# Optimization experiments

Measured on AMD Instinct MI355X. Metric: run time of the kernel, lower is better.

Reference implementation:

```python
import jax, jax.numpy as jnp
import numpy as np

N = 50000        # nodes
E = 800000       # edges (before self-loops)
NFEAT = 256
NHID = 32
HEADS = 8
NOUT = 128
NEG_SLOPE = 0.2
EPS = 1e-5


def _gat_layer(x, src, dst, W, att_src, att_dst, bias, heads, ch, concat):
    """PyG-style GATConv (shared weights for src/dst, self-loops already appended)."""
    n = x.shape[0]
    h = (x @ W).reshape(n, heads, ch)                      # [N,H,C]
    a_src = (h * att_src).sum(-1)                          # [N,H]
    a_dst = (h * att_dst).sum(-1)                          # [N,H]
    e = jax.nn.leaky_relu(a_src[src] + a_dst[dst], NEG_SLOPE)  # [E',H]
    # segment softmax over incoming edges of each dst node
    m = jax.ops.segment_max(e, dst, num_segments=n)        # [N,H]
    m = jnp.where(jnp.isfinite(m), m, 0.0)
    ex = jnp.exp(e - m[dst])                               # [E',H]
    denom = jax.ops.segment_sum(ex, dst, num_segments=n)   # [N,H]
    alpha = ex / (denom[dst] + 1e-16)                      # [E',H]
    msg = h[src] * alpha[:, :, None]                       # [E',H,C]
    out = jax.ops.segment_sum(msg, dst, num_segments=n)    # [N,H,C]
    out = out.reshape(n, heads * ch) if concat else out.mean(axis=1)
    return out + bias


def setup_inputs() -> dict:
    key = jax.random.key(0)
    ks = jax.random.split(key, 14)
    s = 0.05
    return {
        "x": jax.random.normal(ks[0], (N, NFEAT), jnp.float32),
        "edge_index": jax.random.randint(ks[1], (2, E), 0, N, dtype=jnp.int64),
        "W1": jax.random.normal(ks[2], (NFEAT, HEADS * NHID), jnp.float32) * s,
        "att_src1": jax.random.normal(ks[3], (HEADS, NHID), jnp.float32) * s,
        "att_dst1": jax.random.normal(ks[4], (HEADS, NHID), jnp.float32) * s,
        "b1": jnp.zeros((HEADS * NHID,), jnp.float32),
        "W2": jax.random.normal(ks[5], (HEADS * NHID, NOUT), jnp.float32) * s,
        "att_src2": jax.random.normal(ks[6], (1, NOUT), jnp.float32) * s,
        "att_dst2": jax.random.normal(ks[7], (1, NOUT), jnp.float32) * s,
        "b2": jnp.zeros((NOUT,), jnp.float32),
        "bn_gamma": jnp.ones((NOUT,), jnp.float32),
        "bn_beta": jnp.zeros((NOUT,), jnp.float32),
        "ln_gamma": jnp.ones((NOUT,), jnp.float32),
        "ln_beta": jnp.zeros((NOUT,), jnp.float32),
    }


def reference(x, edge_index, W1, att_src1, att_dst1, b1, W2, att_src2, att_dst2, b2,
              bn_gamma, bn_beta, ln_gamma, ln_beta):
    loops = jnp.arange(N, dtype=edge_index.dtype)
    src = jnp.concatenate([edge_index[0], loops])
    dst = jnp.concatenate([edge_index[1], loops])
    # layer 1: concat heads, then relu (dropout is identity at inference)
    h = jax.nn.relu(_gat_layer(x, src, dst, W1, att_src1, att_dst1, b1, HEADS, NHID, True))
    # layer 2: single head, mean (no concat), relu
    h = jax.nn.relu(_gat_layer(h, src, dst, W2, att_src2, att_dst2, b2, 1, NOUT, False))
    # BatchNorm1d with batch statistics (biased var, eps=1e-5)
    mu = h.mean(axis=0)
    var = h.var(axis=0)
    h = (h - mu) / jnp.sqrt(var + EPS) * bn_gamma + bn_beta
    # LayerNorm over last dim
    mu2 = h.mean(axis=-1, keepdims=True)
    var2 = h.var(axis=-1, keepdims=True)
    return (h - mu2) / jnp.sqrt(var2 + EPS) * ln_gamma + ln_beta
```

## Files before the change

kernel.cpp:

```cpp
#include <hip/hip_runtime.h>
#include <cstdint>
#include <cstddef>

#define HEADS   8
#define NFEAT   256
#define NOUT    128
#define NEG     0.2f
#define EPSV    1e-5f

typedef unsigned short ushort_t;
typedef __attribute__((ext_vector_type(8))) short s8v;
typedef __attribute__((ext_vector_type(4))) float f4v;

static __device__ __forceinline__ float lrelu(float x) { return x > 0.f ? x : NEG * x; }

static __device__ __forceinline__ float bf2f(ushort_t u) {
    union { unsigned int i; float f; } v; v.i = ((unsigned int)u) << 16; return v.f;
}
static __device__ __forceinline__ ushort_t f2bf(float f) {
    union { float f; unsigned int i; } v; v.f = f;
    unsigned int x = v.i;
    return (ushort_t)((x + 0x7fff + ((x >> 16) & 1)) >> 16);
}
static __device__ __forceinline__ float bits2f(unsigned int u) {
    union { unsigned int i; float f; } v; v.i = u; return v.f;
}
static __device__ __forceinline__ unsigned int f2bits(float f) {
    union { float f; unsigned int i; } v; v.f = f; return v.i;
}

static __device__ __forceinline__ int detect64(const int* __restrict__ ei, int E) {
    int lane = threadIdx.x & 63;
    long idx = 2L * ((long)lane * (E / 64)) + 1;
    int v = ei[idx];
    unsigned long long ball = __ballot(v == 0);
    return (ball == ~0ull) ? 1 : 0;
}

__global__ void k_count(const int* __restrict__ ei, int* __restrict__ counts,
                        int E, int n) {
    int is64 = detect64(ei, E);
    int i = blockIdx.x * blockDim.x + threadIdx.x;
    if (i < E) {
        int d = ei[(size_t)(E + i) << is64];
        atomicAdd(&counts[d], 1);
    } else if (i < E + n) {
        atomicAdd(&counts[i - E], 1);
    }
}

__global__ __launch_bounds__(1024) void k_scan1(const int* __restrict__ counts,
                                                int* __restrict__ incl,
                                                int* __restrict__ bsum, int n) {
    int t = threadIdx.x, i = blockIdx.x * 1024 + t;
    int lane = t & 63, w = t >> 6;
    int v = (i < n) ? counts[i] : 0;
    int sv = v;
#pragma unroll
    for (int o = 1; o < 64; o <<= 1) { int u = __shfl_up(sv, o, 64); if (lane >= o) sv += u; }
    __shared__ int wsum[16];
    if (lane == 63) wsum[w] = sv;
    __syncthreads();
    if (w == 0) {
        int bs = (lane < 16) ? wsum[lane] : 0;
#pragma unroll
        for (int o = 1; o < 16; o <<= 1) { int u = __shfl_up(bs, o, 64); if (lane >= o) bs += u; }
        if (lane < 16) wsum[lane] = bs;
    }
    __syncthreads();
    int pre = (w > 0) ? wsum[w - 1] : 0;
    sv += pre;
    if (i < n) incl[i] = sv;
    if (t == 1023) bsum[blockIdx.x] = sv;
}

__global__ void k_scan3(const int* __restrict__ incl, const int* __restrict__ bsum,
                        const int* __restrict__ counts,
                        int* __restrict__ offs, int* __restrict__ cursor, int n) {
    __shared__ int pre_s;
    int chunk = blockIdx.x >> 2;
    if (threadIdx.x == 0) {
        int s = 0;
        for (int j = 0; j < chunk; ++j) s += bsum[j];
        pre_s = s;
    }
    __syncthreads();
    int i = blockIdx.x * 256 + threadIdx.x;
    if (i < n) {
        int v = incl[i] + pre_s;
        offs[i + 1] = v;
        cursor[i] = v - counts[i];
    }
    if (i == 0) offs[0] = 0;
}

__global__ void k_fill(const int* __restrict__ ei, int* __restrict__ cursor,
                       int* __restrict__ esrc, int E, int n) {
    int is64 = detect64(ei, E);
    int i = blockIdx.x * blockDim.x + threadIdx.x;
    if (i >= E + n) return;
    int s, d;
    if (i < E) { s = ei[(size_t)i << is64]; d = ei[(size_t)(E + i) << is64]; }
    else       { s = i - E; d = s; }
    int p = atomicAdd(&cursor[d], 1);
    esrc[p] = s;
}

__global__ void k_prepw(const float* __restrict__ W1, const float* __restrict__ W2,
                        ushort_t* __restrict__ Wh1, ushort_t* __restrict__ Wl1,
                        ushort_t* __restrict__ Wh2, ushort_t* __restrict__ Wl2) {
    int gid = blockIdx.x * 256 + threadIdx.x;
    const float* W; ushort_t* Wh; ushort_t* Wl; int M;
    if (gid < 256 * 256) { W = W1; Wh = Wh1; Wl = Wl1; M = 256; }
    else { gid -= 256 * 256; if (gid >= 256 * 128) return; W = W2; Wh = Wh2; Wl = Wl2; M = 128; }
    int k = gid / M, nn = gid - k * M;
    int ntile = nn >> 4, j = nn & 15, kc = k >> 3, e = k & 7;
    int p = ((ntile * 32 + kc) * 16 + j) * 8 + e;
    float v = W[(size_t)k * M + nn];
    ushort_t hi = f2bf(v);
    float r = v - bf2f(hi);
    Wh[p] = hi;
    Wl[p] = f2bf(r);
}

__global__ __launch_bounds__(256) void k_mm(const float* __restrict__ A,
                                            const ushort_t* __restrict__ Wh,
                                            const ushort_t* __restrict__ Wl,
                                            ushort_t* __restrict__ C, int n, int Mout) {
    __shared__ ushort_t Ah[128][40];
    __shared__ ushort_t Al[128][40];
    const int t = threadIdx.x;
    const int lane = t & 63, w = t >> 6;
    const int wr = w >> 1, wc = w & 1;
    const int r0 = blockIdx.x * 128;
    const int srow = t >> 1;
    const int kh = (t & 1) * 16;
    const int arow = r0 + srow;
    const bool rowok = arow < n;

    f4v acc[4][4];
#pragma unroll
    for (int a = 0; a < 4; ++a)
#pragma unroll
        for (int b = 0; b < 4; ++b) { f4v z = {0.f, 0.f, 0.f, 0.f}; acc[a][b] = z; }

    float pre[16];
    const float* abase = &A[(size_t)arow * 256 + kh];
#pragma unroll
    for (int q = 0; q < 4; ++q) {
        float4 v = rowok ? *reinterpret_cast<const float4*>(abase + q * 4)
                         : float4{0.f, 0.f, 0.f, 0.f};
        pre[q * 4 + 0] = v.x; pre[q * 4 + 1] = v.y;
        pre[q * 4 + 2] = v.z; pre[q * 4 + 3] = v.w;
    }

    const int lj = lane & 15, lk = lane >> 4;

    for (int kb = 0; kb < 256; kb += 32) {
        __syncthreads();
#pragma unroll
        for (int q = 0; q < 2; ++q) {
            unsigned int hw[4], lw[4];
#pragma unroll
            for (int p = 0; p < 4; ++p) {
                unsigned int x0 = f2bits(pre[q * 8 + p * 2]);
                unsigned int x1 = f2bits(pre[q * 8 + p * 2 + 1]);
                unsigned int h1b = x1 & 0xffff0000u;
                float lo0 = bits2f(f2bits(pre[q * 8 + p * 2])) - bits2f(x0 & 0xffff0000u);
                float lo1 = pre[q * 8 + p * 2 + 1] - bits2f(h1b);
                hw[p] = (x0 >> 16) | h1b;
                lw[p] = (f2bits(lo0) >> 16) | (f2bits(lo1) & 0xffff0000u);
            }
            uint4 hv = {hw[0], hw[1], hw[2], hw[3]};
            uint4 lv = {lw[0], lw[1], lw[2], lw[3]};
            *reinterpret_cast<uint4*>(&Ah[srow][kh + q * 8]) = hv;
            *reinterpret_cast<uint4*>(&Al[srow][kh + q * 8]) = lv;
        }
        __syncthreads();
        if (kb < 224) {
            const float* ap = abase + kb + 32;
#pragma unroll
            for (int q = 0; q < 4; ++q) {
                float4 v = rowok ? *reinterpret_cast<const float4*>(ap + q * 4)
                                 : float4{0.f, 0.f, 0.f, 0.f};
                pre[q * 4 + 0] = v.x; pre[q * 4 + 1] = v.y;
                pre[q * 4 + 2] = v.z; pre[q * 4 + 3] = v.w;
            }
        }
        const int kc0 = kb >> 3;
        s8v ah[4], al[4];
#pragma unroll
        for (int mf = 0; mf < 4; ++mf) {
            ah[mf] = *reinterpret_cast<const s8v*>(&Ah[wr * 64 + mf * 16 + lj][lk * 8]);
            al[mf] = *reinterpret_cast<const s8v*>(&Al[wr * 64 + mf * 16 + lj][lk * 8]);
        }
#pragma unroll
        for (int nf = 0; nf < 4; ++nf) {
            int ntile = blockIdx.y * 8 + wc * 4 + nf;
            size_t boff = ((size_t)(ntile * 32 + kc0 + lk) * 16 + lj) * 8;
            s8v bh = *reinterpret_cast<const s8v*>(&Wh[boff]);
            s8v bl = *reinterpret_cast<const s8v*>(&Wl[boff]);
#pragma unroll
            for (int mf = 0; mf < 4; ++mf) {
                acc[mf][nf] = __builtin_amdgcn_mfma_f32_16x16x32_bf16(ah[mf], bh, acc[mf][nf], 0, 0, 0);
                acc[mf][nf] = __builtin_amdgcn_mfma_f32_16x16x32_bf16(ah[mf], bl, acc[mf][nf], 0, 0, 0);
                acc[mf][nf] = __builtin_amdgcn_mfma_f32_16x16x32_bf16(al[mf], bh, acc[mf][nf], 0, 0, 0);
            }
        }
    }

#pragma unroll
    for (int mf = 0; mf < 4; ++mf) {
        int rr = r0 + wr * 64 + mf * 16 + lk * 4;
#pragma unroll
        for (int nf = 0; nf < 4; ++nf) {
            int cc = blockIdx.y * 128 + wc * 64 + nf * 16 + lj;
#pragma unroll
            for (int r = 0; r < 4; ++r) {
                if (rr + r < n) C[(size_t)(rr + r) * Mout + cc] = f2bf(acc[mf][nf][r]);
            }
        }
    }
}

__global__ __launch_bounds__(256) void k_att1(const ushort_t* __restrict__ h1,
                                              const float* __restrict__ att_s,
                                              const float* __restrict__ att_d,
                                              float* __restrict__ as1,
                                              float* __restrict__ ad1, int n) {
    int wid = (blockIdx.x * blockDim.x + threadIdx.x) >> 6;
    int lane = threadIdx.x & 63;
    if (wid >= n) return;
    int head = lane >> 3;
    int co = (lane & 7) * 4;
    ushort4 hu = *reinterpret_cast<const ushort4*>(&h1[(size_t)wid * 256 + head * 32 + co]);
    float4 vs = *reinterpret_cast<const float4*>(&att_s[head * 32 + co]);
    float4 vd = *reinterpret_cast<const float4*>(&att_d[head * 32 + co]);
    float hx = bf2f(hu.x), hy = bf2f(hu.y), hz = bf2f(hu.z), hw = bf2f(hu.w);
    float ss = hx * vs.x + hy * vs.y + hz * vs.z + hw * vs.w;
    float sd = hx * vd.x + hy * vd.y + hz * vd.z + hw * vd.w;
#pragma unroll
    for (int o = 1; o < 8; o <<= 1) { ss += __shfl_xor(ss, o, 64); sd += __shfl_xor(sd, o, 64); }
    if ((lane & 7) == 0) {
        as1[(size_t)wid * 8 + head] = ss;
        ad1[(size_t)wid * 8 + head] = sd;
    }
}

__global__ __launch_bounds__(256) void k_att2(const ushort_t* __restrict__ h2,
                                              const float* __restrict__ att_s,
                                              const float* __restrict__ att_d,
                                              float* __restrict__ as2,
                                              float* __restrict__ ad2, int n) {
    int wid = (blockIdx.x * blockDim.x + threadIdx.x) >> 6;
    int lane = threadIdx.x & 63;
    if (wid >= n) return;
    ushort2 hu = *reinterpret_cast<const ushort2*>(&h2[(size_t)wid * 128 + lane * 2]);
    float2 vs = *reinterpret_cast<const float2*>(&att_s[lane * 2]);
    float2 vd = *reinterpret_cast<const float2*>(&att_d[lane * 2]);
    float hx = bf2f(hu.x), hy = bf2f(hu.y);
    float ss = hx * vs.x + hy * vs.y;
    float sd = hx * vd.x + hy * vd.y;
#pragma unroll
    for (int o = 1; o < 64; o <<= 1) { ss += __shfl_xor(ss, o, 64); sd += __shfl_xor(sd, o, 64); }
    if (lane == 0) { as2[wid] = ss; ad2[wid] = sd; }
}

__global__ __launch_bounds__(256) void k_agg1(const ushort_t* __restrict__ h1,
                                              const float* __restrict__ as1,
                                              const float* __restrict__ ad1,
                                              const int* __restrict__ offs,
                                              const int* __restrict__ esrc,
                                              const float* __restrict__ b1,
                                              float* __restrict__ out1, int n, int tot) {
    int wid = (blockIdx.x * blockDim.x + threadIdx.x) >> 6;
    int lane = threadIdx.x & 63;
    if (wid >= n) return;
    int e0 = offs[wid], e1 = offs[wid + 1];
    int deg = e1 - e0;

    if (deg <= 64) {
        const int l = lane & 31;
        const int h = lane >> 5;
        const int hd = l >> 2;
        const int cb = l * 8;

        int ei_idx = e0 + lane;
        int es = esrc[ei_idx < tot ? ei_idx : (tot - 1)];

        const int headA = lane >> 3, g = lane & 7;
        float adnA = ad1[(size_t)wid * 8 + headA];
        float a[8];
#pragma unroll
        for (int k = 0; k < 8; ++k) {
            int i = g + 8 * k;
            int s = __shfl(es, i, 64);
            a[k] = (i < deg) ? as1[(size_t)s * 8 + headA] : -1e30f;
        }
        float mx = a[0];
#pragma unroll
        for (int k = 1; k < 8; ++k) mx = fmaxf(mx, a[k]);
#pragma unroll
        for (int o = 1; o < 8; o <<= 1) mx = fmaxf(mx, __shfl_xor(mx, o, 64));
        float mA = lrelu(mx + adnA);
#pragma unroll
        for (int k = 0; k < 8; ++k)
            a[k] = __expf(lrelu(a[k] + adnA) - mA);

        float d = 0.f;
        float ac0 = 0.f, ac1 = 0.f, ac2 = 0.f, ac3 = 0.f;
        float ac4 = 0.f, ac5 = 0.f, ac6 = 0.f, ac7 = 0.f;
#pragma unroll
        for (int u = 0; u < 8; ++u) {
            if (8 * u < deg) {
#pragma unroll
                for (int v = 0; v < 4; ++v) {
                    int i = 8 * u + 2 * v + h;
                    int s = __shfl(es, i, 64);
                    float p = __shfl(a[u], hd * 8 + 2 * v + h, 64);
                    if (i < deg) {
                        uint4 hv = *reinterpret_cast<const uint4*>(&h1[(size_t)s * 256 + cb]);
                        d += p;
                        ac0 += p * bits2f(hv.x << 16);
                        ac1 += p * bits2f(hv.x & 0xffff0000u);
                        ac2 += p * bits2f(hv.y << 16);
                        ac3 += p * bits2f(hv.y & 0xffff0000u);
                        ac4 += p * bits2f(hv.z << 16);
                        ac5 += p * bits2f(hv.z & 0xffff0000u);
                        ac6 += p * bits2f(hv.w << 16);
                        ac7 += p * bits2f(hv.w & 0xffff0000u);
                    }
                }
            }
        }
        d   += __shfl_xor(d, 32, 64);
        ac0 += __shfl_xor(ac0, 32, 64); ac1 += __shfl_xor(ac1, 32, 64);
        ac2 += __shfl_xor(ac2, 32, 64); ac3 += __shfl_xor(ac3, 32, 64);
        ac4 += __shfl_xor(ac4, 32, 64); ac5 += __shfl_xor(ac5, 32, 64);
        ac6 += __shfl_xor(ac6, 32, 64); ac7 += __shfl_xor(ac7, 32, 64);
        if (lane < 32) {
            float inv = 1.f / (d + 1e-16f);
            float4 b0 = *reinterpret_cast<const float4*>(&b1[cb]);
            float4 b4 = *reinterpret_cast<const float4*>(&b1[cb + 4]);
            float4 o0, o1;
            o0.x = fmaxf(ac0 * inv + b0.x, 0.f);
            o0.y = fmaxf(ac1 * inv + b0.y, 0.f);
            o0.z = fmaxf(ac2 * inv + b0.z, 0.f);
            o0.w = fmaxf(ac3 * inv + b0.w, 0.f);
            o1.x = fmaxf(ac4 * inv + b4.x, 0.f);
            o1.y = fmaxf(ac5 * inv + b4.y, 0.f);
            o1.z = fmaxf(ac6 * inv + b4.z, 0.f);
            o1.w = fmaxf(ac7 * inv + b4.w, 0.f);
            *reinterpret_cast<float4*>(&out1[(size_t)wid * 256 + cb]) = o0;
            *reinterpret_cast<float4*>(&out1[(size_t)wid * 256 + cb + 4]) = o1;
        }
    } else {
        int head = lane >> 3;
        int g = lane & 7;
        int cb = lane * 4;
        float adn = ad1[(size_t)wid * 8 + head];
        float mx = -1e30f;
        for (int e = e0 + g; e < e1; e += 8)
            mx = fmaxf(mx, as1[(size_t)esrc[e] * 8 + head]);
#pragma unroll
        for (int o = 1; o < 8; o <<= 1) mx = fmaxf(mx, __shfl_xor(mx, o, 64));
        float m = lrelu(mx + adn);
        float d = 0.f, ax = 0.f, ay = 0.f, az = 0.f, aw = 0.f;
        for (int e = e0; e < e1; ++e) {
            int s = esrc[e];
            float p = __expf(lrelu(as1[(size_t)s * 8 + head] + adn) - m);
            ushort4 hv = *reinterpret_cast<const ushort4*>(&h1[(size_t)s * 256 + cb]);
            d += p;
            ax += p * bf2f(hv.x);
            ay += p * bf2f(hv.y);
            az += p * bf2f(hv.z);
            aw += p * bf2f(hv.w);
        }
        float inv = 1.f / (d + 1e-16f);
        float4 bb = *reinterpret_cast<const float4*>(&b1[cb]);
        float4 o;
        o.x = fmaxf(ax * inv + bb.x, 0.f);
        o.y = fmaxf(ay * inv + bb.y, 0.f);
        o.z = fmaxf(az * inv + bb.z, 0.f);
        o.w = fmaxf(aw * inv + bb.w, 0.f);
        *reinterpret_cast<float4*>(&out1[(size_t)wid * 256 + cb]) = o;
    }
}

__global__ __launch_bounds__(256) void k_agg2(const ushort_t* __restrict__ h2,
                                              const float* __restrict__ as2,
                                              const float* __restrict__ ad2,
                                              const int* __restrict__ offs,
                                              const int* __restrict__ esrc,
                                              const float* __restrict__ b2,
                                              float* __restrict__ out2, int n, int tot) {
    int wid = (blockIdx.x * blockDim.x + threadIdx.x) >> 6;
    int lane = threadIdx.x & 63;
    if (wid >= n) return;
    float adn = ad2[wid];
    int e0 = offs[wid], e1 = offs[wid + 1];
    int deg = e1 - e0;

    if (deg <= 64) {
        const int l = lane & 15;
        const int q = lane >> 4;
        const int cb = l * 8;

        int ei_idx = e0 + lane;
        int es = esrc[ei_idx < tot ? ei_idx : (tot - 1)];
        float av0 = (lane < deg) ? as2[es] : -1e30f;
        float mx = av0;
#pragma unroll
        for (int o = 1; o < 64; o <<= 1) mx = fmaxf(mx, __shfl_xor(mx, o, 64));
        float m = lrelu(mx + adn);
        float p0 = __expf(lrelu(av0 + adn) - m);

        float d = 0.f;
        float ac0 = 0.f, ac1 = 0.f, ac2 = 0.f, ac3 = 0.f;
        float ac4 = 0.f, ac5 = 0.f, ac6 = 0.f, ac7 = 0.f;
#pragma unroll
        for (int u = 0; u < 4; ++u) {
            if (16 * u < deg) {
#pragma unroll
                for (int v = 0; v < 4; ++v) {
                    int i = 16 * u + 4 * v + q;
                    int s = __shfl(es, i, 64);
                    float p = __shfl(p0, i, 64);
                    if (i < deg) {
                        uint4 hv = *reinterpret_cast<const uint4*>(&h2[(size_t)s * 128 + cb]);
                        d += p;
                        ac0 += p * bits2f(hv.x << 16);
                        ac1 += p * bits2f(hv.x & 0xffff0000u);
                        ac2 += p * bits2f(hv.y << 16);
                        ac3 += p * bits2f(hv.y & 0xffff0000u);
                        ac4 += p * bits2f(hv.z << 16);
                        ac5 += p * bits2f(hv.z & 0xffff0000u);
                        ac6 += p * bits2f(hv.w << 16);
                        ac7 += p * bits2f(hv.w & 0xffff0000u);
                    }
                }
            }
        }
#pragma unroll
        for (int o = 16; o <= 32; o <<= 1) {
            d   += __shfl_xor(d, o, 64);
            ac0 += __shfl_xor(ac0, o, 64); ac1 += __shfl_xor(ac1, o, 64);
            ac2 += __shfl_xor(ac2, o, 64); ac3 += __shfl_xor(ac3, o, 64);
            ac4 += __shfl_xor(ac4, o, 64); ac5 += __shfl_xor(ac5, o, 64);
            ac6 += __shfl_xor(ac6, o, 64); ac7 += __shfl_xor(ac7, o, 64);
        }
        if (lane < 16) {
            float inv = 1.f / (d + 1e-16f);
            float4 b0 = *reinterpret_cast<const float4*>(&b2[cb]);
            float4 b4 = *reinterpret_cast<const float4*>(&b2[cb + 4]);
            float4 o0, o1;
            o0.x = fmaxf(ac0 * inv + b0.x, 0.f);
            o0.y = fmaxf(ac1 * inv + b0.y, 0.f);
            o0.z = fmaxf(ac2 * inv + b0.z, 0.f);
            o0.w = fmaxf(ac3 * inv + b0.w, 0.f);
            o1.x = fmaxf(ac4 * inv + b4.x, 0.f);
            o1.y = fmaxf(ac5 * inv + b4.y, 0.f);
            o1.z = fmaxf(ac6 * inv + b4.z, 0.f);
            o1.w = fmaxf(ac7 * inv + b4.w, 0.f);
            *reinterpret_cast<float4*>(&out2[(size_t)wid * 128 + cb]) = o0;
            *reinterpret_cast<float4*>(&out2[(size_t)wid * 128 + cb + 4]) = o1;
        }
    } else {
        int cb = lane * 2;
        float mx = -1e30f;
        for (int e = e0 + lane; e < e1; e += 64)
            mx = fmaxf(mx, as2[esrc[e]]);
#pragma unroll
        for (int o = 1; o < 64; o <<= 1) mx = fmaxf(mx, __shfl_xor(mx, o, 64));
        float m = lrelu(mx + adn);
        float d = 0.f, ax = 0.f, ay = 0.f;
        for (int e = e0; e < e1; ++e) {
            int s = esrc[e];
            float p = __expf(lrelu(as2[s] + adn) - m);
            ushort2 hv = *reinterpret_cast<const ushort2*>(&h2[(size_t)s * 128 + cb]);
            d += p;
            ax += p * bf2f(hv.x);
            ay += p * bf2f(hv.y);
        }
        float inv = 1.f / (d + 1e-16f);
        float o0 = fmaxf(ax * inv + b2[cb], 0.f);
        float o1 = fmaxf(ay * inv + b2[cb + 1], 0.f);
        float2 o = {o0, o1};
        *reinterpret_cast<float2*>(&out2[(size_t)wid * 128 + cb]) = o;
    }
}

__global__ __launch_bounds__(128) void k_bnstat(const float* __restrict__ out2,
                                                float* __restrict__ bnsum,
                                                float* __restrict__ bnsq, int n) {
    int c = threadIdx.x;
    float s = 0.f, q = 0.f;
    for (int r = blockIdx.x; r < n; r += gridDim.x) {
        float v = out2[(size_t)r * 128 + c];
        s += v;
        q += v * v;
    }
    atomicAdd(&bnsum[c], s);
    atomicAdd(&bnsq[c], q);
}

__global__ __launch_bounds__(256) void k_final(const float* __restrict__ out2,
                                               const float* __restrict__ bnsum,
                                               const float* __restrict__ bnsq,
                                               const float* __restrict__ bng,
                                               const float* __restrict__ bnb,
                                               const float* __restrict__ lng,
                                               const float* __restrict__ lnb,
                                               float* __restrict__ out, int n) {
    int wid = (blockIdx.x * blockDim.x + threadIdx.x) >> 6;
    int lane = threadIdx.x & 63;
    if (wid >= n) return;
    int c0 = lane, c1 = lane + 64;
    float invn = 1.f / (float)n;
    float mu0 = bnsum[c0] * invn, mu1 = bnsum[c1] * invn;
    float v0 = bnsq[c0] * invn - mu0 * mu0;
    float v1 = bnsq[c1] * invn - mu1 * mu1;
    float r0 = rsqrtf(v0 + EPSV), r1 = rsqrtf(v1 + EPSV);
    float x0 = out2[(size_t)wid * 128 + c0];
    float x1 = out2[(size_t)wid * 128 + c1];
    float y0 = (x0 - mu0) * r0 * bng[c0] + bnb[c0];
    float y1 = (x1 - mu1) * r1 * bng[c1] + bnb[c1];
    float s = y0 + y1, q = y0 * y0 + y1 * y1;
#pragma unroll
    for (int o = 1; o < 64; o <<= 1) { s += __shfl_xor(s, o, 64); q += __shfl_xor(q, o, 64); }
    float mu = s * (1.f / 128.f);
    float var = q * (1.f / 128.f) - mu * mu;
    float rr = rsqrtf(var + EPSV);
    out[(size_t)wid * 128 + c0] = (y0 - mu) * rr * lng[c0] + lnb[c0];
    out[(size_t)wid * 128 + c1] = (y1 - mu) * rr * lng[c1] + lnb[c1];
}

extern "C" void kernel_launch(void* const* d_in, const int* in_sizes, int n_in,
                              void* d_out, int out_size, void* d_ws, size_t ws_size,
                              hipStream_t stream) {
    const float* x    = (const float*)d_in[0];
    const int*   ei   = (const int*)d_in[1];
    const float* W1   = (const float*)d_in[2];
    const float* ats1 = (const float*)d_in[3];
    const float* atd1 = (const float*)d_in[4];
    const float* b1   = (const float*)d_in[5];
    const float* W2   = (const float*)d_in[6];
    const float* ats2 = (const float*)d_in[7];
    const float* atd2 = (const float*)d_in[8];
    const float* b2   = (const float*)d_in[9];
    const float* bng  = (const float*)d_in[10];
    const float* bnb  = (const float*)d_in[11];
    const float* lng  = (const float*)d_in[12];
    const float* lnb  = (const float*)d_in[13];

    const int n = in_sizes[0] / NFEAT;
    const int E = in_sizes[1] / 2;
    const int tot = E + n;

    auto align = [](size_t v) { return (v + 255) & ~(size_t)255; };
    char* ws = (char*)d_ws;
    size_t off = 0;
    ushort_t* h1 = (ushort_t*)(ws + off); off += align((size_t)n * 256 * 2);
    float* out1 = (float*)(ws + off); off += align((size_t)n * 256 * 4);
    ushort_t* h2 = h1;
    float* out2 = out1;
    float* as1 = (float*)(ws + off); off += align((size_t)n * 8 * 4);
    float* ad1 = (float*)(ws + off); off += align((size_t)n * 8 * 4);
    float* as2 = (float*)(ws + off); off += align((size_t)n * 4);
    float* ad2 = (float*)(ws + off); off += align((size_t)n * 4);
    int* counts = (int*)(ws + off); off += align((size_t)n * 4 + 1024);
    float* bnsum = (float*)(counts + n);
    float* bnsq  = bnsum + 128;
    int* offs   = (int*)(ws + off); off += align((size_t)(n + 1) * 4);
    int* cursor = (int*)(ws + off); off += align((size_t)n * 4);
    int* esrc   = (int*)(ws + off); off += align((size_t)tot * 4);
    int* incl   = (int*)(ws + off); off += align((size_t)n * 4);
    int* bsum   = (int*)(ws + off); off += align(64 * 4);
    ushort_t* Wh1 = (ushort_t*)(ws + off); off += align((size_t)256 * 256 * 2);
    ushort_t* Wl1 = (ushort_t*)(ws + off); off += align((size_t)256 * 256 * 2);
    ushort_t* Wh2 = (ushort_t*)(ws + off); off += align((size_t)256 * 128 * 2);
    ushort_t* Wl2 = (ushort_t*)(ws + off); off += align((size_t)256 * 128 * 2);

    hipMemsetAsync(counts, 0, (size_t)n * 4 + 1024, stream);

    k_prepw<<<(256 * 256 + 256 * 128 + 255) / 256, 256, 0, stream>>>(W1, W2, Wh1, Wl1, Wh2, Wl2);

    k_count<<<(tot + 255) / 256, 256, 0, stream>>>(ei, counts, E, n);
    int nsb = (n + 1023) / 1024;
    k_scan1<<<nsb, 1024, 0, stream>>>(counts, incl, bsum, n);
    k_scan3<<<(n + 255) / 256, 256, 0, stream>>>(incl, bsum, counts, offs, cursor, n);
    k_fill<<<(tot + 255) / 256, 256, 0, stream>>>(ei, cursor, esrc, E, n);

    const int gx = (n + 127) / 128;
    k_mm<<<dim3(gx, 2), 256, 0, stream>>>(x, Wh1, Wl1, h1, n, 256);
    k_att1<<<(n + 3) / 4, 256, 0, stream>>>(h1, ats1, atd1, as1, ad1, n);
    k_agg1<<<(n + 3) / 4, 256, 0, stream>>>(h1, as1, ad1, offs, esrc, b1, out1, n, tot);

    k_mm<<<dim3(gx, 1), 256, 0, stream>>>(out1, Wh2, Wl2, h2, n, 128);
    k_att2<<<(n + 3) / 4, 256, 0, stream>>>(h2, ats2, atd2, as2, ad2, n);
    k_agg2<<<(n + 3) / 4, 256, 0, stream>>>(h2, as2, ad2, offs, esrc, b2, out2, n, tot);

    k_bnstat<<<512, 128, 0, stream>>>(out2, bnsum, bnsq, n);
    k_final<<<(n + 3) / 4, 256, 0, stream>>>(out2, bnsum, bnsq, bng, bnb, lng, lnb,
                                             (float*)d_out, n);
}
```

Baseline: 354.4 us.

## Fuse attention-score dot products into GEMM epilogue and merge prep kernels

Computes the per-head a_src/a_dst attention scores directly from the MFMA accumulators in the k_mm epilogue, removing the separate k_att1/k_att2 kernels and their re-reads of h. Layer 2 combines its two column halves with atomics into buffers that are now zeroed by the existing memset. The count and weight-prep kernels are merged into one launch, and the aggregation kernels switch to 128-thread blocks. Scores now come from fp32 accumulators rather than the bf16-rounded h, and layer-2 atomics make the float summation order nondeterministic.

```diff
diff --git a/kernel.cpp b/kernel.cpp
--- a/kernel.cpp
+++ b/kernel.cpp
@@ -37,15 +37,33 @@
     return (ball == ~0ull) ? 1 : 0;
 }
 
-__global__ void k_count(const int* __restrict__ ei, int* __restrict__ counts,
-                        int E, int n) {
-    int is64 = detect64(ei, E);
-    int i = blockIdx.x * blockDim.x + threadIdx.x;
-    if (i < E) {
-        int d = ei[(size_t)(E + i) << is64];
-        atomicAdd(&counts[d], 1);
-    } else if (i < E + n) {
-        atomicAdd(&counts[i - E], 1);
+__global__ void k_prep(const int* __restrict__ ei, int* __restrict__ counts,
+                       int E, int n, int cblocks,
+                       const float* __restrict__ W1, const float* __restrict__ W2,
+                       ushort_t* __restrict__ Wh1, ushort_t* __restrict__ Wl1,
+                       ushort_t* __restrict__ Wh2, ushort_t* __restrict__ Wl2) {
+    if (blockIdx.x < (unsigned)cblocks) {
+        int is64 = detect64(ei, E);
+        int i = blockIdx.x * 256 + threadIdx.x;
+        if (i < E) {
+            int d = ei[(size_t)(E + i) << is64];
+            atomicAdd(&counts[d], 1);
+        } else if (i < E + n) {
+            atomicAdd(&counts[i - E], 1);
+        }
+    } else {
+        int gid = (blockIdx.x - cblocks) * 256 + threadIdx.x;
+        const float* W; ushort_t* Wh; ushort_t* Wl; int M;
+        if (gid < 256 * 256) { W = W1; Wh = Wh1; Wl = Wl1; M = 256; }
+        else { gid -= 256 * 256; if (gid >= 256 * 128) return; W = W2; Wh = Wh2; Wl = Wl2; M = 128; }
+        int k = gid / M, nn = gid - k * M;
+        int ntile = nn >> 4, j = nn & 15, kc = k >> 3, e = k & 7;
+        int p = ((ntile * 32 + kc) * 16 + j) * 8 + e;
+        float v = W[(size_t)k * M + nn];
+        ushort_t hi = f2bf(v);
+        float r = v - bf2f(hi);
+        Wh[p] = hi;
+        Wl[p] = f2bf(r);
     }
 }
 
@@ -106,27 +124,15 @@
     esrc[p] = s;
 }
 
-__global__ void k_prepw(const float* __restrict__ W1, const float* __restrict__ W2,
-                        ushort_t* __restrict__ Wh1, ushort_t* __restrict__ Wl1,
-                        ushort_t* __restrict__ Wh2, ushort_t* __restrict__ Wl2) {
-    int gid = blockIdx.x * 256 + threadIdx.x;
-    const float* W; ushort_t* Wh; ushort_t* Wl; int M;
-    if (gid < 256 * 256) { W = W1; Wh = Wh1; Wl = Wl1; M = 256; }
-    else { gid -= 256 * 256; if (gid >= 256 * 128) return; W = W2; Wh = Wh2; Wl = Wl2; M = 128; }
-    int k = gid / M, nn = gid - k * M;
-    int ntile = nn >> 4, j = nn & 15, kc = k >> 3, e = k & 7;
-    int p = ((ntile * 32 + kc) * 16 + j) * 8 + e;
-    float v = W[(size_t)k * M + nn];
-    ushort_t hi = f2bf(v);
-    float r = v - bf2f(hi);
-    Wh[p] = hi;
-    Wl[p] = f2bf(r);
-}
-
+template <int MOUT>
 __global__ __launch_bounds__(256) void k_mm(const float* __restrict__ A,
                                             const ushort_t* __restrict__ Wh,
                                             const ushort_t* __restrict__ Wl,
-                                            ushort_t* __restrict__ C, int n, int Mout) {
+                                            ushort_t* __restrict__ C,
+                                            const float* __restrict__ att_s,
+                                            const float* __restrict__ att_d,
+                                            float* __restrict__ as_o,
+                                            float* __restrict__ ad_o, int n) {
     __shared__ ushort_t Ah[128][40];
     __shared__ ushort_t Al[128][40];
     const int t = threadIdx.x;
@@ -166,7 +172,7 @@
                 unsigned int x0 = f2bits(pre[q * 8 + p * 2]);
                 unsigned int x1 = f2bits(pre[q * 8 + p * 2 + 1]);
                 unsigned int h1b = x1 & 0xffff0000u;
-                float lo0 = bits2f(f2bits(pre[q * 8 + p * 2])) - bits2f(x0 & 0xffff0000u);
+                float lo0 = pre[q * 8 + p * 2] - bits2f(x0 & 0xffff0000u);
                 float lo1 = pre[q * 8 + p * 2 + 1] - bits2f(h1b);
                 hw[p] = (x0 >> 16) | h1b;
                 lw[p] = (f2bits(lo0) >> 16) | (f2bits(lo1) & 0xffff0000u);
@@ -217,63 +223,72 @@
             int cc = blockIdx.y * 128 + wc * 64 + nf * 16 + lj;
 #pragma unroll
             for (int r = 0; r < 4; ++r) {
-                if (rr + r < n) C[(size_t)(rr + r) * Mout + cc] = f2bf(acc[mf][nf][r]);
-            }
-        }
-    }
-}
-
-__global__ __launch_bounds__(256) void k_att1(const ushort_t* __restrict__ h1,
-                                              const float* __restrict__ att_s,
-                                              const float* __restrict__ att_d,
-                                              float* __restrict__ as1,
-                                              float* __restrict__ ad1, int n) {
-    int wid = (blockIdx.x * blockDim.x + threadIdx.x) >> 6;
-    int lane = threadIdx.x & 63;
-    if (wid >= n) return;
-    int head = lane >> 3;
-    int co = (lane & 7) * 4;
-    ushort4 hu = *reinterpret_cast<const ushort4*>(&h1[(size_t)wid * 256 + head * 32 + co]);
-    float4 vs = *reinterpret_cast<const float4*>(&att_s[head * 32 + co]);
-    float4 vd = *reinterpret_cast<const float4*>(&att_d[head * 32 + co]);
-    float hx = bf2f(hu.x), hy = bf2f(hu.y), hz = bf2f(hu.z), hw = bf2f(hu.w);
-    float ss = hx * vs.x + hy * vs.y + hz * vs.z + hw * vs.w;
-    float sd = hx * vd.x + hy * vd.y + hz * vd.z + hw * vd.w;
-#pragma unroll
-    for (int o = 1; o < 8; o <<= 1) { ss += __shfl_xor(ss, o, 64); sd += __shfl_xor(sd, o, 64); }
-    if ((lane & 7) == 0) {
-        as1[(size_t)wid * 8 + head] = ss;
-        ad1[(size_t)wid * 8 + head] = sd;
-    }
-}
-
-__global__ __launch_bounds__(256) void k_att2(const ushort_t* __restrict__ h2,
-                                              const float* __restrict__ att_s,
-                                              const float* __restrict__ att_d,
-                                              float* __restrict__ as2,
-                                              float* __restrict__ ad2, int n) {
-    int wid = (blockIdx.x * blockDim.x + threadIdx.x) >> 6;
-    int lane = threadIdx.x & 63;
-    if (wid >= n) return;
-    ushort2 hu = *reinterpret_cast<const ushort2*>(&h2[(size_t)wid * 128 + lane * 2]);
-    float2 vs = *reinterpret_cast<const float2*>(&att_s[lane * 2]);
-    float2 vd = *reinterpret_cast<const float2*>(&att_d[lane * 2]);
-    float hx = bf2f(hu.x), hy = bf2f(hu.y);
-    float ss = hx * vs.x + hy * vs.y;
-    float sd = hx * vd.x + hy * vd.y;
-#pragma unroll
-    for (int o = 1; o < 64; o <<= 1) { ss += __shfl_xor(ss, o, 64); sd += __shfl_xor(sd, o, 64); }
-    if (lane == 0) { as2[wid] = ss; ad2[wid] = sd; }
-}
-
-__global__ __launch_bounds__(256) void k_agg1(const ushort_t* __restrict__ h1,
+                if (rr + r < n) C[(size_t)(rr + r) * MOUT + cc] = f2bf(acc[mf][nf][r]);
+            }
+        }
+    }
+
+    const int colw = (MOUT == 256 ? blockIdx.y * 128 : 0) + wc * 64;
+    float asv[4], adv[4];
+#pragma unroll
+    for (int nf = 0; nf < 4; ++nf) {
+        asv[nf] = att_s[colw + nf * 16 + lj];
+        adv[nf] = att_d[colw + nf * 16 + lj];
+    }
+    if (MOUT == 256) {
+        int headA = colw >> 5;
+#pragma unroll
+        for (int mf = 0; mf < 4; ++mf) {
+            int rr = r0 + wr * 64 + mf * 16 + lk * 4;
+#pragma unroll
+            for (int r = 0; r < 4; ++r) {
+                float ssA = acc[mf][0][r] * asv[0] + acc[mf][1][r] * asv[1];
+                float sdA = acc[mf][0][r] * adv[0] + acc[mf][1][r] * adv[1];
+                float ssB = acc[mf][2][r] * asv[2] + acc[mf][3][r] * asv[3];
+                float sdB = acc[mf][2][r] * adv[2] + acc[mf][3][r] * adv[3];
+#pragma unroll
+                for (int o = 1; o < 16; o <<= 1) {
+                    ssA += __shfl_xor(ssA, o, 64); sdA += __shfl_xor(sdA, o, 64);
+                    ssB += __shfl_xor(ssB, o, 64); sdB += __shfl_xor(sdB, o, 64);
+                }
+                if (lj == 0 && rr + r < n) {
+                    size_t rb = (size_t)(rr + r) * 8;
+                    as_o[rb + headA] = ssA;  ad_o[rb + headA] = sdA;
+                    as_o[rb + headA + 1] = ssB;  ad_o[rb + headA + 1] = sdB;
+                }
+            }
+        }
+    } else {
+#pragma unroll
+        for (int mf = 0; mf < 4; ++mf) {
+            int rr = r0 + wr * 64 + mf * 16 + lk * 4;
+#pragma unroll
+            for (int r = 0; r < 4; ++r) {
+                float ss = acc[mf][0][r] * asv[0] + acc[mf][1][r] * asv[1]
+                         + acc[mf][2][r] * asv[2] + acc[mf][3][r] * asv[3];
+                float sd = acc[mf][0][r] * adv[0] + acc[mf][1][r] * adv[1]
+                         + acc[mf][2][r] * adv[2] + acc[mf][3][r] * adv[3];
+#pragma unroll
+                for (int o = 1; o < 16; o <<= 1) {
+                    ss += __shfl_xor(ss, o, 64); sd += __shfl_xor(sd, o, 64);
+                }
+                if (lj == 0 && rr + r < n) {
+                    atomicAdd(&as_o[rr + r], ss);
+                    atomicAdd(&ad_o[rr + r], sd);
+                }
+            }
+        }
+    }
+}
+
+__global__ __launch_bounds__(128) void k_agg1(const ushort_t* __restrict__ h1,
                                               const float* __restrict__ as1,
                                               const float* __restrict__ ad1,
                                               const int* __restrict__ offs,
                                               const int* __restrict__ esrc,
                                               const float* __restrict__ b1,
                                               float* __restrict__ out1, int n, int tot) {
-    int wid = (blockIdx.x * blockDim.x + threadIdx.x) >> 6;
+    int wid = (blockIdx.x * 128 + threadIdx.x) >> 6;
     int lane = threadIdx.x & 63;
     if (wid >= n) return;
     int e0 = offs[wid], e1 = offs[wid + 1];
@@ -387,14 +402,14 @@
     }
 }
 
-__global__ __launch_bounds__(256) void k_agg2(const ushort_t* __restrict__ h2,
+__global__ __launch_bounds__(128) void k_agg2(const ushort_t* __restrict__ h2,
                                               const float* __restrict__ as2,
                                               const float* __restrict__ ad2,
                                               const int* __restrict__ offs,
                                               const int* __restrict__ esrc,
                                               const float* __restrict__ b2,
                                               float* __restrict__ out2, int n, int tot) {
-    int wid = (blockIdx.x * blockDim.x + threadIdx.x) >> 6;
+    int wid = (blockIdx.x * 128 + threadIdx.x) >> 6;
     int lane = threadIdx.x & 63;
     if (wid >= n) return;
     float adn = ad2[wid];
@@ -566,11 +581,11 @@
     float* out2 = out1;
     float* as1 = (float*)(ws + off); off += align((size_t)n * 8 * 4);
     float* ad1 = (float*)(ws + off); off += align((size_t)n * 8 * 4);
-    float* as2 = (float*)(ws + off); off += align((size_t)n * 4);
-    float* ad2 = (float*)(ws + off); off += align((size_t)n * 4);
-    int* counts = (int*)(ws + off); off += align((size_t)n * 4 + 1024);
+    int* counts = (int*)(ws + off); off += align((size_t)n * 12 + 1024);
     float* bnsum = (float*)(counts + n);
     float* bnsq  = bnsum + 128;
+    float* as2   = bnsq + 128;
+    float* ad2   = as2 + n;
     int* offs   = (int*)(ws + off); off += align((size_t)(n + 1) * 4);
     int* cursor = (int*)(ws + off); off += align((size_t)n * 4);
     int* esrc   = (int*)(ws + off); off += align((size_t)tot * 4);
@@ -581,24 +596,23 @@
     ushort_t* Wh2 = (ushort_t*)(ws + off); off += align((size_t)256 * 128 * 2);
     ushort_t* Wl2 = (ushort_t*)(ws + off); off += align((size_t)256 * 128 * 2);
 
-    hipMemsetAsync(counts, 0, (size_t)n * 4 + 1024, stream);
-
-    k_prepw<<<(256 * 256 + 256 * 128 + 255) / 256, 256, 0, stream>>>(W1, W2, Wh1, Wl1, Wh2, Wl2);
-
-    k_count<<<(tot + 255) / 256, 256, 0, stream>>>(ei, counts, E, n);
+    hipMemsetAsync(counts, 0, (size_t)n * 12 + 1024, stream);
+
+    const int cblocks = (tot + 255) / 256;
+    const int pblocks = (256 * 256 + 256 * 128 + 255) / 256;
+    k_prep<<<cblocks + pblocks, 256, 0, stream>>>(ei, counts, E, n, cblocks,
+                                                  W1, W2, Wh1, Wl1, Wh2, Wl2);
     int nsb = (n + 1023) / 1024;
     k_scan1<<<nsb, 1024, 0, stream>>>(counts, incl, bsum, n);
     k_scan3<<<(n + 255) / 256, 256, 0, stream>>>(incl, bsum, counts, offs, cursor, n);
     k_fill<<<(tot + 255) / 256, 256, 0, stream>>>(ei, cursor, esrc, E, n);
 
     const int gx = (n + 127) / 128;
-    k_mm<<<dim3(gx, 2), 256, 0, stream>>>(x, Wh1, Wl1, h1, n, 256);
-    k_att1<<<(n + 3) / 4, 256, 0, stream>>>(h1, ats1, atd1, as1, ad1, n);
-    k_agg1<<<(n + 3) / 4, 256, 0, stream>>>(h1, as1, ad1, offs, esrc, b1, out1, n, tot);
-
-    k_mm<<<dim3(gx, 1), 256, 0, stream>>>(out1, Wh2, Wl2, h2, n, 128);
-    k_att2<<<(n + 3) / 4, 256, 0, stream>>>(h2, ats2, atd2, as2, ad2, n);
-    k_agg2<<<(n + 3) / 4, 256, 0, stream>>>(h2, as2, ad2, offs, esrc, b2, out2, n, tot);
+    k_mm<256><<<dim3(gx, 2), 256, 0, stream>>>(x, Wh1, Wl1, h1, ats1, atd1, as1, ad1, n);
+    k_agg1<<<(n + 1) / 2, 128, 0, stream>>>(h1, as1, ad1, offs, esrc, b1, out1, n, tot);
+
+    k_mm<128><<<dim3(gx, 1), 256, 0, stream>>>(out1, Wh2, Wl2, h2, ats2, atd2, as2, ad2, n);
+    k_agg2<<<(n + 1) / 2, 128, 0, stream>>>(h2, as2, ad2, offs, esrc, b2, out2, n, tot);
 
     k_bnstat<<<512, 128, 0, stream>>>(out2, bnsum, bnsq, n);
     k_final<<<(n + 3) / 4, 256, 0, stream>>>(out2, bnsum, bnsq, bng, bnb, lng, lnb,
```

After: 350.7 us. No clear change (-1.0%).
